# Kernel optimization log

Hardware: AMD Instinct MI355X
Metric: run time of the kernel (lower is better)

## Reference

```python
import jax, jax.numpy as jnp
import numpy as np

GRID_SIZE = 8
MARGIN = 1.0
NUM_NEG = 4
SOS_NEG = 8
LOSS_LAMBDA = 1.0
IMG_H, IMG_W = 960, 1280  # desc2 is the stride-GRID_SIZE feature map of this image
BIG = 5.0    # fill for radius-masked entries in FOS distance matrix (> max unit-desc dist 2)
HUGE = 1e6   # fill for invalid entries in SOS candidate scores


def _l2n(x, eps=1e-8):
    return x / (jnp.linalg.norm(x, axis=-1, keepdims=True) + eps)


def _pdist(a, b, eps=1e-12):
    # a: B x N x C, b: B x M x C -> B x N x M euclidean distances
    sq = (jnp.sum(a * a, -1)[..., :, None] + jnp.sum(b * b, -1)[..., None, :]
          - 2.0 * jnp.einsum('bnc,bmc->bnm', a, b))
    return jnp.sqrt(jnp.maximum(sq, eps))


def _bilinear(desc, pts):
    # desc: B x C x H x W, pts: B x N x 2 in (y, x) image-pixel coords -> B x N x C
    B, C, H, W = desc.shape
    g = pts / GRID_SIZE - 0.5  # image coords -> feature-grid coords
    gy = jnp.clip(g[..., 0], 0.0, H - 1.0)
    gx = jnp.clip(g[..., 1], 0.0, W - 1.0)
    y0 = jnp.clip(jnp.floor(gy).astype(jnp.int32), 0, H - 2)
    x0 = jnp.clip(jnp.floor(gx).astype(jnp.int32), 0, W - 2)
    wy = (gy - y0)[:, None, :]
    wx = (gx - x0)[:, None, :]
    flat = desc.reshape(B, C, H * W)
    gat = lambda yi, xi: jnp.take_along_axis(flat, (yi * W + xi)[:, None, :], axis=2)
    v00, v01 = gat(y0, x0), gat(y0, x0 + 1)
    v10, v11 = gat(y0 + 1, x0), gat(y0 + 1, x0 + 1)
    out = (v00 * (1 - wy) * (1 - wx) + v01 * (1 - wy) * wx
           + v10 * wy * (1 - wx) + v11 * wy * wx)
    return out.transpose(0, 2, 1)


def _forward(kp1, w_kp1, kp1_desc, desc2, homo12):
    r = 2.0 * GRID_SIZE  # spatial masking radius
    d1 = _l2n(kp1_desc)                       # B x N x C
    w_desc = _l2n(_bilinear(desc2, w_kp1))    # B x N x C interpolated warped descriptors

    # visibility of kp1 under homography homo12 (kp stored as (y, x))
    ones = jnp.ones_like(kp1[..., :1])
    p = jnp.concatenate([kp1[..., 1:2], kp1[..., 0:1], ones], -1)  # (x, y, 1)
    q = jnp.einsum('bij,bnj->bni', homo12, p)
    qx = q[..., 0] / (q[..., 2] + 1e-8)
    qy = q[..., 1] / (q[..., 2] + 1e-8)
    vis = ((qx >= 0) & (qx < IMG_W) & (qy >= 0) & (qy < IMG_H)).astype(d1.dtype)
    denom = jnp.sum(vis) + 1e-8

    # ---- FOS: hard quad triplet with radius masking ----
    pos = jnp.sqrt(jnp.sum((d1 - w_desc) ** 2, -1) + 1e-12)  # B x N
    D = _pdist(d1, w_desc)          # B x N x N cross descriptor distances
    s22 = _pdist(w_kp1, w_kp1)      # B x N x N warped-coordinate distances
    Dm = jnp.where(s22 <= r, BIG, D)  # mask spatial near-positives (incl. diagonal)
    neg1 = -jax.lax.top_k(-Dm, NUM_NEG)[0]                       # hardest negs per row anchor
    neg2 = -jax.lax.top_k(-Dm.transpose(0, 2, 1), NUM_NEG)[0]    # per column anchor
    t1 = jnp.mean(jax.nn.relu(MARGIN + pos[..., None] - neg1), -1)
    t2 = jnp.mean(jax.nn.relu(MARGIN + pos[..., None] - neg2), -1)
    fos = jnp.sum(vis * 0.5 * (t1 + t2)) / denom

    # ---- SOS: radius-masked second-order similarity regularizer ----
    s11 = _pdist(kp1, kp1)
    d11 = _pdist(d1, d1)
    d22 = _pdist(w_desc, w_desc)
    valid = (s11 > r) & (s22 > r)
    score = jnp.where(valid, d11, HUGE)
    nscore, idx = jax.lax.top_k(-score, SOS_NEG)  # sos_neg hardest valid neighbors
    sel_d11 = -nscore
    sel_d22 = jnp.take_along_axis(d22, idx, axis=2)
    diff2 = jnp.where(sel_d11 < HUGE * 0.1, (sel_d11 - sel_d22) ** 2, 0.0)
    sos_i = jnp.sqrt(jnp.sum(diff2, -1) + 1e-12)
    sos = jnp.sum(vis * sos_i) / denom

    return (fos + sos) * LOSS_LAMBDA


def setup_inputs() -> dict:
    key = jax.random.key(0)
    k1, k2, k3, k4, k5 = jax.random.split(key, 5)
    B, N, C, H, W = 2, 4096, 128, 120, 160
    scale = jnp.array([IMG_H - 1.0, IMG_W - 1.0], dtype=jnp.float32)
    kp1 = jax.random.uniform(k1, (B, N, 2), dtype=jnp.float32) * scale
    w_kp1 = jax.random.uniform(k2, (B, N, 2), dtype=jnp.float32) * scale
    kp1_desc = jax.random.normal(k3, (B, N, C), dtype=jnp.float32)
    desc2 = jax.random.normal(k4, (B, C, H, W), dtype=jnp.float32)
    homo12 = (jnp.tile(jnp.eye(3, dtype=jnp.float32), (B, 1, 1))
              + 0.001 * jax.random.normal(k5, (B, 3, 3), dtype=jnp.float32))
    return {'kp1': kp1, 'w_kp1': w_kp1, 'kp1_desc': kp1_desc,
            'desc2': desc2, 'homo12': homo12}


def reference(kp1, w_kp1, kp1_desc, desc2, homo12):
    return _forward(kp1, w_kp1, kp1_desc, desc2, homo12)
```

## Files before the change

### kernel.cpp

```cpp
#include <hip/hip_runtime.h>
#include <hip/hip_fp16.h>
#include <math.h>

#define NPTS 4096
#define CDIM 128
#define FH 120
#define FW 160
#define PIX (FH * FW)

typedef __attribute__((ext_vector_type(8))) short short8_t;
typedef __attribute__((ext_vector_type(4))) float float4_t;
typedef __attribute__((ext_vector_type(2))) unsigned short ushort2_t;

#define OFF_FRAG  0
#define OFF_WDB   1048576
#define OFF_JA    1572864
#define OFF_JB    1605632
#define OFF_POS   1622016
#define OFF_VIS   1630208
#define OFF_ACC   1638400
#define OFF_PARTS 1638416
#define OFF_D2T   2031632
#define OFF_END   4489232

__device__ __forceinline__ unsigned short f2bf(float f) {
  unsigned int u = __float_as_uint(f);
  u = (u + 0x7fffu + ((u >> 16) & 1u)) >> 16;
  return (unsigned short)u;
}

__device__ __forceinline__ float wavesum(float v) {
#pragma unroll
  for (int off = 1; off < 64; off <<= 1) v += __shfl_xor(v, off, 64);
  return v;
}

__global__ __launch_bounds__(256) void transpose_desc2(
    const float* __restrict__ d2, unsigned short* __restrict__ out) {
  __shared__ unsigned short tile[64][130];
  const int bp = blockIdx.x;
  const int b = bp / 300;
  const int p0 = (bp - b * 300) * 64;
  const int tid = threadIdx.x;
  const int grp = tid >> 6, lp = tid & 63;
#pragma unroll 4
  for (int r = 0; r < 32; ++r) {
    int c = (r << 2) | grp;
    float v = d2[((size_t)b * CDIM + c) * PIX + p0 + lp];
    tile[lp][c] = __half_as_ushort(__float2half(v));
  }
  __syncthreads();
  unsigned int* ob = (unsigned int*)(out + ((size_t)b * PIX + p0) * CDIM);
#pragma unroll
  for (int i = 0; i < 16; ++i) {
    int u = (i << 8) | tid;
    int p = u >> 6, cc = (u & 63) << 1;
    unsigned int lo = tile[p][cc], hi = tile[p][cc + 1];
    ob[u] = lo | (hi << 16);
  }
}

#define PREP_TAIL() do {                                                        \
  {                                                                             \
    const int T = (p & (NPTS - 1)) >> 4, cRow = p & 15;                         \
    const int kcL = lane >> 4, quadL = (lane >> 2) & 3, jjL = (lane & 3) * 2;   \
    const size_t off = (size_t)(quadL * 16 + cRow) * 8 + jjL;                   \
    const size_t tb = (((size_t)b * 256 + T) * 2) * 4;                          \
    ushort2_t st; st.x = f2bf(d0); st.y = f2bf(d1v);                            \
    ushort2_t sw; sw.x = f2bf(e0); sw.y = f2bf(e1);                             \
    *(ushort2_t*)(frag + (tb + kcL) * 512 + off) = st;                          \
    *(ushort2_t*)(frag + (tb + 4 + kcL) * 512 + off) = sw;                      \
    ushort2_t swr; swr.x = f2bf(e0); swr.y = f2bf(e1);                          \
    *(ushort2_t*)(wdb + (size_t)p * CDIM + c2) = swr;                           \
  }                                                                             \
  float dd0 = d0 - e0, dd1 = d1v - e1;                                          \
  float ssp = wavesum(dd0 * dd0 + dd1 * dd1);                                   \
  if (lane == 0) {                                                              \
    pos[p] = sqrtf(ssp + 1e-12f);                                               \
    float ky = kp1[p * 2 + 0], kx = kp1[p * 2 + 1];                             \
    jA[p] = make_float4(ky, kx, y, x);                                          \
    jB[p] = make_float2(n1, n2);                                                \
    const float* h = homo + b * 9;                                              \
    float t0 = h[0] * kx + h[1] * ky + h[2];                                    \
    float t1 = h[3] * kx + h[4] * ky + h[5];                                    \
    float t2 = h[6] * kx + h[7] * ky + h[8];                                    \
    float qx = t0 / (t2 + 1e-8f), qy = t1 / (t2 + 1e-8f);                       \
    vis[p] = (qx >= 0.0f && qx < 1280.0f && qy >= 0.0f && qy < 960.0f)          \
                 ? 1.0f : 0.0f;                                                 \
  }                                                                             \
} while (0)

__global__ __launch_bounds__(256) void prep_t(
    const float* __restrict__ kp1, const float* __restrict__ wkp1,
    const float* __restrict__ desc, const unsigned short* __restrict__ d2t,
    const float* __restrict__ homo,
    unsigned short* __restrict__ frag, unsigned short* __restrict__ wdb,
    float4* __restrict__ jA, float2* __restrict__ jB,
    float* __restrict__ pos, float* __restrict__ vis, float* __restrict__ acc) {
  const int tid = threadIdx.x;
  if (blockIdx.x == 0 && tid < 4) acc[tid] = 0.0f;
  const int p = blockIdx.x * 4 + (tid >> 6);
  const int lane = tid & 63;
  const int b = p >> 12;
  const int c2 = lane * 2;

  float2 v = *(const float2*)(desc + (size_t)p * CDIM + c2);
  float ss = wavesum(v.x * v.x + v.y * v.y);
  float inv = 1.0f / (sqrtf(ss) + 1e-8f);
  float d0 = v.x * inv, d1v = v.y * inv;
  float n1 = ss * inv * inv;

  float y = wkp1[p * 2 + 0], x = wkp1[p * 2 + 1];
  float gy = fminf(fmaxf(y * 0.125f - 0.5f, 0.0f), (float)(FH - 1));
  float gx = fminf(fmaxf(x * 0.125f - 0.5f, 0.0f), (float)(FW - 1));
  int y0 = (int)floorf(gy); y0 = min(max(y0, 0), FH - 2);
  int x0 = (int)floorf(gx); x0 = min(max(x0, 0), FW - 2);
  float wy = gy - (float)y0, wx = gx - (float)x0;
  float w00 = (1 - wy) * (1 - wx), w01 = (1 - wy) * wx;
  float w10 = wy * (1 - wx), w11 = wy * wx;
  const unsigned int* t00 = (const unsigned int*)
      (d2t + ((size_t)b * PIX + y0 * FW + x0) * CDIM) + lane;
  unsigned int u00 = t00[0], u01 = t00[64];
  unsigned int u10 = t00[FW * 64], u11 = t00[FW * 64 + 64];
  float2 f00 = __half22float2(*(const __half2*)&u00);
  float2 f01 = __half22float2(*(const __half2*)&u01);
  float2 f10 = __half22float2(*(const __half2*)&u10);
  float2 f11 = __half22float2(*(const __half2*)&u11);
  float wv0 = f00.x * w00 + f01.x * w01 + f10.x * w10 + f11.x * w11;
  float wv1 = f00.y * w00 + f01.y * w01 + f10.y * w10 + f11.y * w11;
  float ss2 = wavesum(wv0 * wv0 + wv1 * wv1);
  float inv2 = 1.0f / (sqrtf(ss2) + 1e-8f);
  float e0 = wv0 * inv2, e1 = wv1 * inv2;
  float n2 = ss2 * inv2 * inv2;

  PREP_TAIL();
}

__global__ __launch_bounds__(256) void prep_g(
    const float* __restrict__ kp1, const float* __restrict__ wkp1,
    const float* __restrict__ desc, const float* __restrict__ desc2,
    const float* __restrict__ homo,
    unsigned short* __restrict__ frag, unsigned short* __restrict__ wdb,
    float4* __restrict__ jA, float2* __restrict__ jB,
    float* __restrict__ pos, float* __restrict__ vis, float* __restrict__ acc) {
  const int tid = threadIdx.x;
  if (blockIdx.x == 0 && tid < 4) acc[tid] = 0.0f;
  const int p = blockIdx.x * 4 + (tid >> 6);
  const int lane = tid & 63;
  const int b = p >> 12;
  const int c2 = lane * 2;

  float2 v = *(const float2*)(desc + (size_t)p * CDIM + c2);
  float ss = wavesum(v.x * v.x + v.y * v.y);
  float inv = 1.0f / (sqrtf(ss) + 1e-8f);
  float d0 = v.x * inv, d1v = v.y * inv;
  float n1 = ss * inv * inv;

  float y = wkp1[p * 2 + 0], x = wkp1[p * 2 + 1];
  float gy = fminf(fmaxf(y * 0.125f - 0.5f, 0.0f), (float)(FH - 1));
  float gx = fminf(fmaxf(x * 0.125f - 0.5f, 0.0f), (float)(FW - 1));
  int y0 = (int)floorf(gy); y0 = min(max(y0, 0), FH - 2);
  int x0 = (int)floorf(gx); x0 = min(max(x0, 0), FW - 2);
  float wy = gy - (float)y0, wx = gx - (float)x0;
  float w00 = (1 - wy) * (1 - wx), w01 = (1 - wy) * wx;
  float w10 = wy * (1 - wx), w11 = wy * wx;
  const float* q0 = desc2 + ((size_t)b * CDIM + c2) * PIX + y0 * FW + x0;
  const float* q1 = q0 + PIX;
  float wv0 = q0[0] * w00 + q0[1] * w01 + q0[FW] * w10 + q0[FW + 1] * w11;
  float wv1 = q1[0] * w00 + q1[1] * w01 + q1[FW] * w10 + q1[FW + 1] * w11;
  float ss2 = wavesum(wv0 * wv0 + wv1 * wv1);
  float inv2 = 1.0f / (sqrtf(ss2) + 1e-8f);
  float e0 = wv0 * inv2, e1 = wv1 * inv2;
  float n2 = ss2 * inv2 * inv2;

  PREP_TAIL();
}

__device__ __forceinline__ void ins4m(float v, float* L) {
  float p0 = L[0]; L[0] = fmaxf(L[0], v);
  float p1 = L[1]; L[1] = __builtin_amdgcn_fmed3f(p0, L[1], v);
  float p2 = L[2]; L[2] = __builtin_amdgcn_fmed3f(p1, L[2], v);
  L[3] = __builtin_amdgcn_fmed3f(p2, L[3], v);
}
__device__ __forceinline__ void ins6m(float v, float* L) {
  float p0 = L[0]; L[0] = fmaxf(L[0], v);
  float p1 = L[1]; L[1] = __builtin_amdgcn_fmed3f(p0, L[1], v);
  float p2 = L[2]; L[2] = __builtin_amdgcn_fmed3f(p1, L[2], v);
  float p3 = L[3]; L[3] = __builtin_amdgcn_fmed3f(p2, L[3], v);
  float p4 = L[4]; L[4] = __builtin_amdgcn_fmed3f(p3, L[4], v);
  L[5] = __builtin_amdgcn_fmed3f(p4, L[5], v);
}
__device__ __forceinline__ void ins10m(float v, float* L) {
  float p0 = L[0]; L[0] = fmaxf(L[0], v);
  float pk = p0;
#pragma unroll
  for (int k = 1; k < 9; ++k) {
    float cur = L[k];
    L[k] = __builtin_amdgcn_fmed3f(pk, cur, v);
    pk = cur;
  }
  L[9] = __builtin_amdgcn_fmed3f(pk, L[9], v);
}

__device__ __forceinline__ float packkey(float s, int j) {
  return __uint_as_float((__float_as_uint(s) & 0xFFFFF000u) | (unsigned)j);
}

#define TILE_COMPUTE(AD, AW, NA, NB, J0) do {                                   \
  float4_t aD = {0,0,0,0}, aDt = {0,0,0,0}, a11 = {0,0,0,0};                    \
  _Pragma("unroll")                                                             \
  for (int kc = 0; kc < 4; ++kc) {                                              \
    aD  = __builtin_amdgcn_mfma_f32_16x16x32_bf16(AW[kc], Bd[kc], aD,  0,0,0);  \
    aDt = __builtin_amdgcn_mfma_f32_16x16x32_bf16(AD[kc], Bw[kc], aDt, 0,0,0);  \
    a11 = __builtin_amdgcn_mfma_f32_16x16x32_bf16(AD[kc], Bd[kc], a11, 0,0,0);  \
  }                                                                             \
  const float nj1[4] = {NA.x, NA.z, NB.x, NB.z};                                \
  const float nj2[4] = {NA.y, NA.w, NB.y, NB.w};                                \
  _Pragma("unroll")                                                             \
  for (int reg = 0; reg < 4; ++reg) {                                           \
    const int jj = (J0) + (quad << 2) + reg;                                    \
    ins4m(packkey(fmaf(2.0f, aD[reg],  -nj2[reg]), jj), fD);                    \
    ins4m(packkey(fmaf(2.0f, aDt[reg], -nj1[reg]), jj), fDt);                   \
    ins6m(packkey(fmaf(2.0f, a11[reg], -nj1[reg]), jj), fS);                    \
  }                                                                             \
} while (0)

__global__ __launch_bounds__(256, 3) void loss_main(
    const unsigned short* __restrict__ frag,
    const float2* __restrict__ jBg, float* __restrict__ parts) {
  __shared__ float mb[4][16][24];

  const int tid = threadIdx.x;
  const int bid = blockIdx.x;
  const int b = bid & 1;
  const int half = (bid >> 1) & 1;
  const int g = bid >> 2;
  const int i0 = g * 16;
  const int wave = tid >> 6, lane = tid & 63;
  const int c = lane & 15, quad = lane >> 4;
  const int base = b * NPTS;

  short8_t Bd[4], Bw[4];
  {
    const unsigned short* fb = frag + ((((size_t)b * 256 + g) * 2) * 4) * 512 + (size_t)lane * 8;
#pragma unroll
    for (int kc = 0; kc < 4; ++kc) {
      Bd[kc] = *(const short8_t*)(fb + kc * 512);
      Bw[kc] = *(const short8_t*)(fb + (4 + kc) * 512);
    }
  }

  float fD[4], fDt[4], fS[6];
#pragma unroll
  for (int k = 0; k < 4; ++k) { fD[k] = -1e30f; fDt[k] = -1e30f; }
#pragma unroll
  for (int k = 0; k < 6; ++k) fS[k] = -1e30f;

  const int jstart = (half << 11) | (wave << 9);
  const unsigned short* fa = frag + (((size_t)b * 256 + (jstart >> 4)) * 8) * 512 + (size_t)lane * 8;
  const float2* jbb = jBg + base;

  short8_t A0d[4], A0w[4], A1d[4], A1w[4];
#pragma unroll
  for (int kc = 0; kc < 4; ++kc) {
    A0d[kc] = *(const short8_t*)(fa + kc * 512);
    A0w[kc] = *(const short8_t*)(fa + (4 + kc) * 512);
  }
  float4 n0a = *(const float4*)(jbb + jstart + (quad << 2));
  float4 n0b = *(const float4*)(jbb + jstart + (quad << 2) + 2);
  float4 n1a, n1b;

  for (int t = 0; t < 32; t += 2) {
    const unsigned short* f1 = fa + 4096;
#pragma unroll
    for (int kc = 0; kc < 4; ++kc) {
      A1d[kc] = *(const short8_t*)(f1 + kc * 512);
      A1w[kc] = *(const short8_t*)(f1 + (4 + kc) * 512);
    }
    {
      const int j1 = jstart + ((t + 1) << 4);
      n1a = *(const float4*)(jbb + j1 + (quad << 2));
      n1b = *(const float4*)(jbb + j1 + (quad << 2) + 2);
    }
    TILE_COMPUTE(A0d, A0w, n0a, n0b, jstart + (t << 4));
    const unsigned short* f2 = fa + ((t + 2 < 32) ? 8192 : 0);
#pragma unroll
    for (int kc = 0; kc < 4; ++kc) {
      A0d[kc] = *(const short8_t*)(f2 + kc * 512);
      A0w[kc] = *(const short8_t*)(f2 + (4 + kc) * 512);
    }
    {
      const int j2 = jstart + (((t + 2) & 31) << 4);
      n0a = *(const float4*)(jbb + j2 + (quad << 2));
      n0b = *(const float4*)(jbb + j2 + (quad << 2) + 2);
    }
    TILE_COMPUTE(A1d, A1w, n1a, n1b, jstart + ((t + 1) << 4));
    fa += 8192;
  }

  float eD[6], eDt[6], eS[10];
#pragma unroll
  for (int k = 0; k < 4; ++k) { eD[k] = fD[k]; eDt[k] = fDt[k]; }
  eD[4] = eD[5] = eDt[4] = eDt[5] = -1e30f;
#pragma unroll
  for (int k = 0; k < 6; ++k) eS[k] = fS[k];
  eS[6] = eS[7] = eS[8] = eS[9] = -1e30f;

  {
    float tmp[10];
#pragma unroll
    for (int off = 16; off <= 32; off <<= 1) {
#pragma unroll
      for (int k = 0; k < 6; ++k) tmp[k] = eD[k];
#pragma unroll
      for (int k = 0; k < 6; ++k) ins6m(__shfl_xor(tmp[k], off, 64), eD);
#pragma unroll
      for (int k = 0; k < 6; ++k) tmp[k] = eDt[k];
#pragma unroll
      for (int k = 0; k < 6; ++k) ins6m(__shfl_xor(tmp[k], off, 64), eDt);
#pragma unroll
      for (int k = 0; k < 10; ++k) tmp[k] = eS[k];
#pragma unroll
      for (int k = 0; k < 10; ++k) ins10m(__shfl_xor(tmp[k], off, 64), eS);
    }
  }

#pragma unroll
  for (int h2 = 2; h2 >= 1; h2 >>= 1) {
    if (wave >= h2 && wave < 2 * h2 && lane < 16) {
      float* m = &mb[wave][lane][0];
#pragma unroll
      for (int k = 0; k < 6; ++k) { m[k] = eD[k]; m[6 + k] = eDt[k]; }
#pragma unroll
      for (int k = 0; k < 10; ++k) m[12 + k] = eS[k];
    }
    __syncthreads();
    if (wave < h2 && lane < 16) {
      const float* m = &mb[wave + h2][lane][0];
#pragma unroll
      for (int k = 0; k < 6; ++k) ins6m(m[k], eD);
#pragma unroll
      for (int k = 0; k < 6; ++k) ins6m(m[6 + k], eDt);
#pragma unroll
      for (int k = 0; k < 10; ++k) ins10m(m[12 + k], eS);
    }
  }

  if (wave == 0 && lane < 16) {
    float* P = parts + (size_t)(half * 24) * 8192 + (base + i0 + lane);
#pragma unroll
    for (int k = 0; k < 6; ++k) {
      P[(size_t)k * 8192] = eD[k];
      P[(size_t)(6 + k) * 8192] = eDt[k];
    }
#pragma unroll
    for (int k = 0; k < 10; ++k) P[(size_t)(12 + k) * 8192] = eS[k];
  }
}

__device__ __forceinline__ float bflo(unsigned int u) { return __uint_as_float(u << 16); }
__device__ __forceinline__ float bfhi(unsigned int u) { return __uint_as_float(u & 0xFFFF0000u); }

__global__ __launch_bounds__(256) void merge_filter(
    const float* __restrict__ parts, const float4* __restrict__ jAg,
    const float2* __restrict__ jBg, const float* __restrict__ posg,
    const float* __restrict__ visg, const unsigned short* __restrict__ wdb,
    float* __restrict__ accum, float* __restrict__ out) {
  __shared__ int sJ[256];
  __shared__ float sD11[256], sD22[256], sFos[32], sVis[32], sN2[32];
  const int tid = threadIdx.x;
  const int a0 = blockIdx.x * 32;

  if (tid < 32) {
    const int a = a0 + tid;
    const int base = a & ~(NPTS - 1);
    float fD[6], fDt[6], fS[10];
    const float* P = parts + a;
#pragma unroll
    for (int k = 0; k < 6; ++k) { fD[k] = P[(size_t)k * 8192]; fDt[k] = P[(size_t)(6 + k) * 8192]; }
#pragma unroll
    for (int k = 0; k < 10; ++k) fS[k] = P[(size_t)(12 + k) * 8192];
    {
      const float* Q = P + (size_t)24 * 8192;
#pragma unroll
      for (int k = 0; k < 6; ++k) {
        ins6m(Q[(size_t)k * 8192], fD);
        ins6m(Q[(size_t)(6 + k) * 8192], fDt);
      }
#pragma unroll
      for (int k = 0; k < 10; ++k) ins10m(Q[(size_t)(12 + k) * 8192], fS);
    }

    const float4 own = jAg[a];
    const float2 nb = jBg[a];
    const float pv = posg[a], vv = visg[a];
    float t1s = 0.0f, t2s = 0.0f;
    int got = 0;
#pragma unroll
    for (int k = 0; k < 6; ++k) {
      int j = (int)(__float_as_uint(fD[k]) & 0xFFFu);
      float4 jc = jAg[base + j];
      float dz = own.z - jc.z, dw = own.w - jc.w;
      if (got < 4 && dz * dz + dw * dw > 256.0f) {
        float d2 = nb.x - fD[k];
        t1s += fmaxf(1.0f + pv - sqrtf(fmaxf(d2, 1e-12f)), 0.0f);
        got++;
      }
    }
    got = 0;
#pragma unroll
    for (int k = 0; k < 6; ++k) {
      int j = (int)(__float_as_uint(fDt[k]) & 0xFFFu);
      float4 jc = jAg[base + j];
      float dz = own.z - jc.z, dw = own.w - jc.w;
      if (got < 4 && dz * dz + dw * dw > 256.0f) {
        float d2 = nb.y - fDt[k];
        t2s += fmaxf(1.0f + pv - sqrtf(fmaxf(d2, 1e-12f)), 0.0f);
        got++;
      }
    }
    int m = 0;
#pragma unroll
    for (int k = 0; k < 10; ++k) {
      int j = (int)(__float_as_uint(fS[k]) & 0xFFFu);
      float4 jc = jAg[base + j];
      float ay = own.x - jc.x, ax = own.y - jc.y;
      float wz = own.z - jc.z, ww = own.w - jc.w;
      if (m < 8 && ay * ay + ax * ax > 256.0f && wz * wz + ww * ww > 256.0f) {
        sJ[tid * 8 + m] = base + j;
        sD11[tid * 8 + m] = sqrtf(fmaxf(nb.x - fS[k], 1e-12f));
        m++;
      }
    }
    for (int k = m; k < 8; ++k) sJ[tid * 8 + k] = -1;
    sFos[tid] = vv * 0.125f * (t1s + t2s);
    sVis[tid] = vv;
    sN2[tid] = nb.y;
  }
  __syncthreads();

  {
    const int slot = tid;
    const int al = slot >> 3;
    const int j = sJ[slot];
    float d22 = 0.0f;
    if (j >= 0) {
      const uint4* pi = (const uint4*)(wdb + (size_t)(a0 + al) * CDIM);
      const uint4* pj = (const uint4*)(wdb + (size_t)j * CDIM);
      float dot = 0.0f;
#pragma unroll
      for (int qq = 0; qq < 16; ++qq) {
        uint4 ui = pi[qq], uj = pj[qq];
        dot = fmaf(bflo(ui.x), bflo(uj.x), dot); dot = fmaf(bfhi(ui.x), bfhi(uj.x), dot);
        dot = fmaf(bflo(ui.y), bflo(uj.y), dot); dot = fmaf(bfhi(ui.y), bfhi(uj.y), dot);
        dot = fmaf(bflo(ui.z), bflo(uj.z), dot); dot = fmaf(bfhi(ui.z), bfhi(uj.z), dot);
        dot = fmaf(bflo(ui.w), bflo(uj.w), dot); dot = fmaf(bfhi(ui.w), bfhi(uj.w), dot);
      }
      d22 = sqrtf(fmaxf(sN2[al] + jBg[j].y - 2.0f * dot, 1e-12f));
    }
    sD22[slot] = d22;
  }
  __syncthreads();

  float contrib = 0.0f, vsum = 0.0f;
  if (tid < 32) {
    float s = 0.0f;
#pragma unroll
    for (int k = 0; k < 8; ++k) {
      if (sJ[tid * 8 + k] >= 0) {
        float d = sD11[tid * 8 + k] - sD22[tid * 8 + k];
        s = fmaf(d, d, s);
      }
    }
    contrib = sFos[tid] + sVis[tid] * sqrtf(s + 1e-12f);
    vsum = sVis[tid];
  }
  if (tid < 64) {
#pragma unroll
    for (int off = 32; off >= 1; off >>= 1) {
      contrib += __shfl_down(contrib, off, 64);
      vsum += __shfl_down(vsum, off, 64);
    }
    if (tid == 0) {
      atomicAdd(&accum[0], contrib);
      atomicAdd(&accum[1], vsum);
      __threadfence();
      float old = atomicAdd(&accum[2], 1.0f);
      if (old == 255.0f) {
        float t = atomicAdd(&accum[0], 0.0f);
        float v = atomicAdd(&accum[1], 0.0f);
        out[0] = t / (v + 1e-8f);
      }
    }
  }
}

extern "C" void kernel_launch(void* const* d_in, const int* in_sizes, int n_in,
                              void* d_out, int out_size, void* d_ws, size_t ws_size,
                              hipStream_t stream) {
  (void)in_sizes; (void)n_in; (void)out_size;
  const float* kp1   = (const float*)d_in[0];
  const float* wkp1  = (const float*)d_in[1];
  const float* desc  = (const float*)d_in[2];
  const float* desc2 = (const float*)d_in[3];
  const float* homo  = (const float*)d_in[4];
  float* ws = (float*)d_ws;
  unsigned short* frag = (unsigned short*)(ws + OFF_FRAG);
  unsigned short* wdb  = (unsigned short*)(ws + OFF_WDB);
  float4* jA = (float4*)(ws + OFF_JA);
  float2* jB = (float2*)(ws + OFF_JB);
  float* pos = ws + OFF_POS;
  float* vis = ws + OFF_VIS;
  float* acc = ws + OFF_ACC;
  float* parts = ws + OFF_PARTS;
  unsigned short* d2t = (unsigned short*)(ws + OFF_D2T);

  if (ws_size >= (size_t)OFF_END * 4) {
    transpose_desc2<<<600, 256, 0, stream>>>(desc2, d2t);
    prep_t<<<2048, 256, 0, stream>>>(kp1, wkp1, desc, d2t, homo,
                                     frag, wdb, jA, jB, pos, vis, acc);
  } else {
    prep_g<<<2048, 256, 0, stream>>>(kp1, wkp1, desc, desc2, homo,
                                     frag, wdb, jA, jB, pos, vis, acc);
  }
  loss_main<<<1024, 256, 0, stream>>>(frag, jB, parts);
  merge_filter<<<256, 256, 0, stream>>>(parts, jA, jB, pos, vis, wdb, acc,
                                        (float*)d_out);
}
```

Measured before the change: 169.5 us.

## Fuse merge into loss_main with last-arriver reduction and LDS double-buffered j-tiles

The main kernel now splits the j dimension into 8 segments per 64-row group. Each block stages the shared j-fragment tiles into LDS through global_load_lds DMA with a double buffer, where before every wave read them straight from global memory. The cross-wave LDS merge and the separate merge_filter launch are removed. A per-tile atomic counter lets the last segment to finish merge all partial top-k lists and run the filter and SOS work inline, which saves a kernel launch and lets tiles share loaded fragments. In exchange it adds a __syncthreads per tile, more partial-result traffic (8 segments), serialized tail work in the last-arriving blocks, and a change of occupancy hint from 3 to 4.

```diff
diff --git a/kernel.cpp b/kernel.cpp
--- a/kernel.cpp
+++ b/kernel.cpp
@@ -7,6 +7,7 @@
 #define FH 120
 #define FW 160
 #define PIX (FH * FW)
+#define SEGS 8
 
 typedef __attribute__((ext_vector_type(8))) short short8_t;
 typedef __attribute__((ext_vector_type(4))) float float4_t;
@@ -19,9 +20,17 @@
 #define OFF_POS   1622016
 #define OFF_VIS   1630208
 #define OFF_ACC   1638400
-#define OFF_PARTS 1638416
-#define OFF_D2T   2031632
-#define OFF_END   4489232
+#define OFF_CNT   1638416
+#define OFF_PARTS 1638928
+#define OFF_D2T   3080720
+#define OFF_END   4309520
+
+typedef const __attribute__((address_space(1))) unsigned int* gas_ptr_t;
+typedef __attribute__((address_space(3))) unsigned int* las_ptr_t;
+
+__device__ __forceinline__ void dma16(const void* g, void* l) {
+  __builtin_amdgcn_global_load_lds((gas_ptr_t)g, (las_ptr_t)l, 16, 0, 0);
+}
 
 __device__ __forceinline__ unsigned short f2bf(float f) {
   unsigned int u = __float_as_uint(f);
@@ -90,15 +99,21 @@
   }                                                                             \
 } while (0)
 
+#define PREP_INIT() do {                                                        \
+  if (blockIdx.x < 2) cnt[blockIdx.x * 256 + tid] = 0;                          \
+  if (blockIdx.x == 2 && tid < 8) acc[tid] = 0.0f;                              \
+} while (0)
+
 __global__ __launch_bounds__(256) void prep_t(
     const float* __restrict__ kp1, const float* __restrict__ wkp1,
     const float* __restrict__ desc, const unsigned short* __restrict__ d2t,
     const float* __restrict__ homo,
     unsigned short* __restrict__ frag, unsigned short* __restrict__ wdb,
     float4* __restrict__ jA, float2* __restrict__ jB,
-    float* __restrict__ pos, float* __restrict__ vis, float* __restrict__ acc) {
+    float* __restrict__ pos, float* __restrict__ vis,
+    float* __restrict__ acc, int* __restrict__ cnt) {
   const int tid = threadIdx.x;
-  if (blockIdx.x == 0 && tid < 4) acc[tid] = 0.0f;
+  PREP_INIT();
   const int p = blockIdx.x * 4 + (tid >> 6);
   const int lane = tid & 63;
   const int b = p >> 12;
@@ -142,9 +157,10 @@
     const float* __restrict__ homo,
     unsigned short* __restrict__ frag, unsigned short* __restrict__ wdb,
     float4* __restrict__ jA, float2* __restrict__ jB,
-    float* __restrict__ pos, float* __restrict__ vis, float* __restrict__ acc) {
+    float* __restrict__ pos, float* __restrict__ vis,
+    float* __restrict__ acc, int* __restrict__ cnt) {
   const int tid = threadIdx.x;
-  if (blockIdx.x == 0 && tid < 4) acc[tid] = 0.0f;
+  PREP_INIT();
   const int p = blockIdx.x * 4 + (tid >> 6);
   const int lane = tid & 63;
   const int b = p >> 12;
@@ -206,43 +222,32 @@
   return __uint_as_float((__float_as_uint(s) & 0xFFFFF000u) | (unsigned)j);
 }
 
-#define TILE_COMPUTE(AD, AW, NA, NB, J0) do {                                   \
-  float4_t aD = {0,0,0,0}, aDt = {0,0,0,0}, a11 = {0,0,0,0};                    \
-  _Pragma("unroll")                                                             \
-  for (int kc = 0; kc < 4; ++kc) {                                              \
-    aD  = __builtin_amdgcn_mfma_f32_16x16x32_bf16(AW[kc], Bd[kc], aD,  0,0,0);  \
-    aDt = __builtin_amdgcn_mfma_f32_16x16x32_bf16(AD[kc], Bw[kc], aDt, 0,0,0);  \
-    a11 = __builtin_amdgcn_mfma_f32_16x16x32_bf16(AD[kc], Bd[kc], a11, 0,0,0);  \
-  }                                                                             \
-  const float nj1[4] = {NA.x, NA.z, NB.x, NB.z};                                \
-  const float nj2[4] = {NA.y, NA.w, NB.y, NB.w};                                \
-  _Pragma("unroll")                                                             \
-  for (int reg = 0; reg < 4; ++reg) {                                           \
-    const int jj = (J0) + (quad << 2) + reg;                                    \
-    ins4m(packkey(fmaf(2.0f, aD[reg],  -nj2[reg]), jj), fD);                    \
-    ins4m(packkey(fmaf(2.0f, aDt[reg], -nj1[reg]), jj), fDt);                   \
-    ins6m(packkey(fmaf(2.0f, a11[reg], -nj1[reg]), jj), fS);                    \
-  }                                                                             \
-} while (0)
-
-__global__ __launch_bounds__(256, 3) void loss_main(
+__device__ __forceinline__ float bflo(unsigned int u) { return __uint_as_float(u << 16); }
+__device__ __forceinline__ float bfhi(unsigned int u) { return __uint_as_float(u & 0xFFFF0000u); }
+
+__global__ __launch_bounds__(256, 4) void loss_main(
     const unsigned short* __restrict__ frag,
-    const float2* __restrict__ jBg, float* __restrict__ parts) {
-  __shared__ float mb[4][16][24];
+    const float4* __restrict__ jAg, const float2* __restrict__ jBg,
+    const float* __restrict__ posg, const float* __restrict__ visg,
+    const unsigned short* __restrict__ wdb,
+    float* __restrict__ parts, int* __restrict__ cnt,
+    float* __restrict__ accum, float* __restrict__ out) {
+  __shared__ char ldsA[2][8192];
 
   const int tid = threadIdx.x;
   const int bid = blockIdx.x;
   const int b = bid & 1;
-  const int half = (bid >> 1) & 1;
-  const int g = bid >> 2;
-  const int i0 = g * 16;
+  const int seg = (bid >> 1) & 7;
+  const int grp = bid >> 4;
   const int wave = tid >> 6, lane = tid & 63;
-  const int c = lane & 15, quad = lane >> 4;
+  const int atile = grp * 4 + wave;
+  const int i0 = atile * 16;
+  const int quad = lane >> 4;
   const int base = b * NPTS;
 
   short8_t Bd[4], Bw[4];
   {
-    const unsigned short* fb = frag + ((((size_t)b * 256 + g) * 2) * 4) * 512 + (size_t)lane * 8;
+    const unsigned short* fb = frag + (((size_t)b * 256 + atile) * 8) * 512 + (size_t)lane * 8;
 #pragma unroll
     for (int kc = 0; kc < 4; ++kc) {
       Bd[kc] = *(const short8_t*)(fb + kc * 512);
@@ -256,46 +261,57 @@
 #pragma unroll
   for (int k = 0; k < 6; ++k) fS[k] = -1e30f;
 
-  const int jstart = (half << 11) | (wave << 9);
-  const unsigned short* fa = frag + (((size_t)b * 256 + (jstart >> 4)) * 8) * 512 + (size_t)lane * 8;
-  const float2* jbb = jBg + base;
-
-  short8_t A0d[4], A0w[4], A1d[4], A1w[4];
-#pragma unroll
-  for (int kc = 0; kc < 4; ++kc) {
-    A0d[kc] = *(const short8_t*)(fa + kc * 512);
-    A0w[kc] = *(const short8_t*)(fa + (4 + kc) * 512);
-  }
-  float4 n0a = *(const float4*)(jbb + jstart + (quad << 2));
-  float4 n0b = *(const float4*)(jbb + jstart + (quad << 2) + 2);
-  float4 n1a, n1b;
-
-  for (int t = 0; t < 32; t += 2) {
-    const unsigned short* f1 = fa + 4096;
+  const int jstart = seg << 9;
+  const unsigned short* ft = frag + (((size_t)b * 256 + (jstart >> 4)) * 8) * 512;
+
+  {
+    const unsigned short* tb0 = ft;
+#pragma unroll
+    for (int ch = 0; ch < 2; ++ch) {
+      int chunk = wave * 2 + ch;
+      dma16(tb0 + chunk * 512 + lane * 8, &ldsA[0][chunk * 1024]);
+    }
+  }
+  __syncthreads();
+
+  for (int t = 0; t < 32; ++t) {
+    const int cur = t & 1;
+    if (t + 1 < 32) {
+      const unsigned short* tbn = ft + (size_t)(t + 1) * 4096;
+#pragma unroll
+      for (int ch = 0; ch < 2; ++ch) {
+        int chunk = wave * 2 + ch;
+        dma16(tbn + chunk * 512 + lane * 8, &ldsA[cur ^ 1][chunk * 1024]);
+      }
+    }
+    const char* lb = &ldsA[cur][0];
+    short8_t Ad[4], Aw[4];
 #pragma unroll
     for (int kc = 0; kc < 4; ++kc) {
-      A1d[kc] = *(const short8_t*)(f1 + kc * 512);
-      A1w[kc] = *(const short8_t*)(f1 + (4 + kc) * 512);
-    }
-    {
-      const int j1 = jstart + ((t + 1) << 4);
-      n1a = *(const float4*)(jbb + j1 + (quad << 2));
-      n1b = *(const float4*)(jbb + j1 + (quad << 2) + 2);
-    }
-    TILE_COMPUTE(A0d, A0w, n0a, n0b, jstart + (t << 4));
-    const unsigned short* f2 = fa + ((t + 2 < 32) ? 8192 : 0);
+      Ad[kc] = *(const short8_t*)(lb + kc * 1024 + lane * 16);
+      Aw[kc] = *(const short8_t*)(lb + (4 + kc) * 1024 + lane * 16);
+    }
+    const int j0 = jstart + (t << 4);
+    const float4 nA = *(const float4*)(jBg + base + j0 + (quad << 2));
+    const float4 nB = *(const float4*)(jBg + base + j0 + (quad << 2) + 2);
+
+    float4_t aD = {0, 0, 0, 0}, aDt = {0, 0, 0, 0}, a11 = {0, 0, 0, 0};
 #pragma unroll
     for (int kc = 0; kc < 4; ++kc) {
-      A0d[kc] = *(const short8_t*)(f2 + kc * 512);
-      A0w[kc] = *(const short8_t*)(f2 + (4 + kc) * 512);
-    }
-    {
-      const int j2 = jstart + (((t + 2) & 31) << 4);
-      n0a = *(const float4*)(jbb + j2 + (quad << 2));
-      n0b = *(const float4*)(jbb + j2 + (quad << 2) + 2);
-    }
-    TILE_COMPUTE(A1d, A1w, n1a, n1b, jstart + ((t + 1) << 4));
-    fa += 8192;
+      aD  = __builtin_amdgcn_mfma_f32_16x16x32_bf16(Aw[kc], Bd[kc], aD,  0, 0, 0);
+      aDt = __builtin_amdgcn_mfma_f32_16x16x32_bf16(Ad[kc], Bw[kc], aDt, 0, 0, 0);
+      a11 = __builtin_amdgcn_mfma_f32_16x16x32_bf16(Ad[kc], Bd[kc], a11, 0, 0, 0);
+    }
+    const float nj1[4] = {nA.x, nA.z, nB.x, nB.z};
+    const float nj2[4] = {nA.y, nA.w, nB.y, nB.w};
+#pragma unroll
+    for (int reg = 0; reg < 4; ++reg) {
+      const int jj = j0 + (quad << 2) + reg;
+      ins4m(packkey(fmaf(2.0f, aD[reg],  -nj2[reg]), jj), fD);
+      ins4m(packkey(fmaf(2.0f, aDt[reg], -nj1[reg]), jj), fDt);
+      ins6m(packkey(fmaf(2.0f, a11[reg], -nj1[reg]), jj), fS);
+    }
+    __syncthreads();
   }
 
   float eD[6], eDt[6], eS[10];
@@ -305,7 +321,6 @@
 #pragma unroll
   for (int k = 0; k < 6; ++k) eS[k] = fS[k];
   eS[6] = eS[7] = eS[8] = eS[9] = -1e30f;
-
   {
     float tmp[10];
 #pragma unroll
@@ -325,29 +340,9 @@
     }
   }
 
-#pragma unroll
-  for (int h2 = 2; h2 >= 1; h2 >>= 1) {
-    if (wave >= h2 && wave < 2 * h2 && lane < 16) {
-      float* m = &mb[wave][lane][0];
-#pragma unroll
-      for (int k = 0; k < 6; ++k) { m[k] = eD[k]; m[6 + k] = eDt[k]; }
-#pragma unroll
-      for (int k = 0; k < 10; ++k) m[12 + k] = eS[k];
-    }
-    __syncthreads();
-    if (wave < h2 && lane < 16) {
-      const float* m = &mb[wave + h2][lane][0];
-#pragma unroll
-      for (int k = 0; k < 6; ++k) ins6m(m[k], eD);
-#pragma unroll
-      for (int k = 0; k < 6; ++k) ins6m(m[6 + k], eDt);
-#pragma unroll
-      for (int k = 0; k < 10; ++k) ins10m(m[12 + k], eS);
-    }
-  }
-
-  if (wave == 0 && lane < 16) {
-    float* P = parts + (size_t)(half * 24) * 8192 + (base + i0 + lane);
+  if (lane < 16) {
+    const int a = base + i0 + lane;
+    float* P = parts + (size_t)(seg * 22) * 8192 + a;
 #pragma unroll
     for (int k = 0; k < 6; ++k) {
       P[(size_t)k * 8192] = eD[k];
@@ -356,41 +351,35 @@
 #pragma unroll
     for (int k = 0; k < 10; ++k) P[(size_t)(12 + k) * 8192] = eS[k];
   }
-}
-
-__device__ __forceinline__ float bflo(unsigned int u) { return __uint_as_float(u << 16); }
-__device__ __forceinline__ float bfhi(unsigned int u) { return __uint_as_float(u & 0xFFFF0000u); }
-
-__global__ __launch_bounds__(256) void merge_filter(
-    const float* __restrict__ parts, const float4* __restrict__ jAg,
-    const float2* __restrict__ jBg, const float* __restrict__ posg,
-    const float* __restrict__ visg, const unsigned short* __restrict__ wdb,
-    float* __restrict__ accum, float* __restrict__ out) {
-  __shared__ int sJ[256];
-  __shared__ float sD11[256], sD22[256], sFos[32], sVis[32], sN2[32];
-  const int tid = threadIdx.x;
-  const int a0 = blockIdx.x * 32;
-
-  if (tid < 32) {
-    const int a = a0 + tid;
-    const int base = a & ~(NPTS - 1);
-    float fD[6], fDt[6], fS[10];
-    const float* P = parts + a;
-#pragma unroll
-    for (int k = 0; k < 6; ++k) { fD[k] = P[(size_t)k * 8192]; fDt[k] = P[(size_t)(6 + k) * 8192]; }
-#pragma unroll
-    for (int k = 0; k < 10; ++k) fS[k] = P[(size_t)(12 + k) * 8192];
-    {
-      const float* Q = P + (size_t)24 * 8192;
+  __threadfence();
+  int old = 0;
+  if (lane == 0) old = atomicAdd(&cnt[b * 256 + atile], 1);
+  old = __shfl(old, 0, 64);
+  if (old != SEGS - 1) return;
+  __threadfence();
+
+  char* scr = &ldsA[0][wave * 2048];
+  int*   sJ   = (int*)scr;
+  float* sD11 = (float*)(scr + 512);
+  float* sD22 = (float*)(scr + 1024);
+  float* sN2  = (float*)(scr + 1536);
+  float* sFv  = (float*)(scr + 1600);
+  float* sVv  = (float*)(scr + 1664);
+
+  if (lane < 16) {
+    const int a = base + i0 + lane;
+#pragma unroll
+    for (int s = 0; s < SEGS; ++s) {
+      if (s == seg) continue;
+      const float* Q = parts + (size_t)(s * 22) * 8192 + a;
 #pragma unroll
       for (int k = 0; k < 6; ++k) {
-        ins6m(Q[(size_t)k * 8192], fD);
-        ins6m(Q[(size_t)(6 + k) * 8192], fDt);
-      }
-#pragma unroll
-      for (int k = 0; k < 10; ++k) ins10m(Q[(size_t)(12 + k) * 8192], fS);
-    }
-
+        ins6m(Q[(size_t)k * 8192], eD);
+        ins6m(Q[(size_t)(6 + k) * 8192], eDt);
+      }
+#pragma unroll
+      for (int k = 0; k < 10; ++k) ins10m(Q[(size_t)(12 + k) * 8192], eS);
+    }
     const float4 own = jAg[a];
     const float2 nb = jBg[a];
     const float pv = posg[a], vv = visg[a];
@@ -398,11 +387,11 @@
     int got = 0;
 #pragma unroll
     for (int k = 0; k < 6; ++k) {
-      int j = (int)(__float_as_uint(fD[k]) & 0xFFFu);
+      int j = (int)(__float_as_uint(eD[k]) & 0xFFFu);
       float4 jc = jAg[base + j];
       float dz = own.z - jc.z, dw = own.w - jc.w;
       if (got < 4 && dz * dz + dw * dw > 256.0f) {
-        float d2 = nb.x - fD[k];
+        float d2 = nb.x - eD[k];
         t1s += fmaxf(1.0f + pv - sqrtf(fmaxf(d2, 1e-12f)), 0.0f);
         got++;
       }
@@ -410,11 +399,11 @@
     got = 0;
 #pragma unroll
     for (int k = 0; k < 6; ++k) {
-      int j = (int)(__float_as_uint(fDt[k]) & 0xFFFu);
+      int j = (int)(__float_as_uint(eDt[k]) & 0xFFFu);
       float4 jc = jAg[base + j];
       float dz = own.z - jc.z, dw = own.w - jc.w;
       if (got < 4 && dz * dz + dw * dw > 256.0f) {
-        float d2 = nb.y - fDt[k];
+        float d2 = nb.y - eDt[k];
         t2s += fmaxf(1.0f + pv - sqrtf(fmaxf(d2, 1e-12f)), 0.0f);
         got++;
       }
@@ -422,30 +411,31 @@
     int m = 0;
 #pragma unroll
     for (int k = 0; k < 10; ++k) {
-      int j = (int)(__float_as_uint(fS[k]) & 0xFFFu);
+      int j = (int)(__float_as_uint(eS[k]) & 0xFFFu);
       float4 jc = jAg[base + j];
       float ay = own.x - jc.x, ax = own.y - jc.y;
       float wz = own.z - jc.z, ww = own.w - jc.w;
       if (m < 8 && ay * ay + ax * ax > 256.0f && wz * wz + ww * ww > 256.0f) {
-        sJ[tid * 8 + m] = base + j;
-        sD11[tid * 8 + m] = sqrtf(fmaxf(nb.x - fS[k], 1e-12f));
+        sJ[lane * 8 + m] = base + j;
+        sD11[lane * 8 + m] = sqrtf(fmaxf(nb.x - eS[k], 1e-12f));
         m++;
       }
     }
-    for (int k = m; k < 8; ++k) sJ[tid * 8 + k] = -1;
-    sFos[tid] = vv * 0.125f * (t1s + t2s);
-    sVis[tid] = vv;
-    sN2[tid] = nb.y;
-  }
-  __syncthreads();
-
-  {
-    const int slot = tid;
+    for (int k = m; k < 8; ++k) sJ[lane * 8 + k] = -1;
+    sFv[lane] = vv * 0.125f * (t1s + t2s);
+    sVv[lane] = vv;
+    sN2[lane] = nb.y;
+  }
+  asm volatile("" ::: "memory");
+
+#pragma unroll
+  for (int rep = 0; rep < 2; ++rep) {
+    const int slot = lane + rep * 64;
     const int al = slot >> 3;
     const int j = sJ[slot];
     float d22 = 0.0f;
     if (j >= 0) {
-      const uint4* pi = (const uint4*)(wdb + (size_t)(a0 + al) * CDIM);
+      const uint4* pi = (const uint4*)(wdb + (size_t)(base + i0 + al) * CDIM);
       const uint4* pj = (const uint4*)(wdb + (size_t)j * CDIM);
       float dot = 0.0f;
 #pragma unroll
@@ -460,37 +450,35 @@
     }
     sD22[slot] = d22;
   }
-  __syncthreads();
+  asm volatile("" ::: "memory");
 
   float contrib = 0.0f, vsum = 0.0f;
-  if (tid < 32) {
+  if (lane < 16) {
     float s = 0.0f;
 #pragma unroll
     for (int k = 0; k < 8; ++k) {
-      if (sJ[tid * 8 + k] >= 0) {
-        float d = sD11[tid * 8 + k] - sD22[tid * 8 + k];
+      if (sJ[lane * 8 + k] >= 0) {
+        float d = sD11[lane * 8 + k] - sD22[lane * 8 + k];
         s = fmaf(d, d, s);
       }
     }
-    contrib = sFos[tid] + sVis[tid] * sqrtf(s + 1e-12f);
-    vsum = sVis[tid];
-  }
-  if (tid < 64) {
-#pragma unroll
-    for (int off = 32; off >= 1; off >>= 1) {
-      contrib += __shfl_down(contrib, off, 64);
-      vsum += __shfl_down(vsum, off, 64);
-    }
-    if (tid == 0) {
-      atomicAdd(&accum[0], contrib);
-      atomicAdd(&accum[1], vsum);
-      __threadfence();
-      float old = atomicAdd(&accum[2], 1.0f);
-      if (old == 255.0f) {
-        float t = atomicAdd(&accum[0], 0.0f);
-        float v = atomicAdd(&accum[1], 0.0f);
-        out[0] = t / (v + 1e-8f);
-      }
+    contrib = sFv[lane] + sVv[lane] * sqrtf(s + 1e-12f);
+    vsum = sVv[lane];
+  }
+#pragma unroll
+  for (int off = 8; off >= 1; off >>= 1) {
+    contrib += __shfl_down(contrib, off, 64);
+    vsum += __shfl_down(vsum, off, 64);
+  }
+  if (lane == 0) {
+    atomicAdd(&accum[0], contrib);
+    atomicAdd(&accum[1], vsum);
+    __threadfence();
+    float o2 = atomicAdd(&accum[2], 1.0f);
+    if (o2 == 511.0f) {
+      float tt = atomicAdd(&accum[0], 0.0f);
+      float vv2 = atomicAdd(&accum[1], 0.0f);
+      out[0] = tt / (vv2 + 1e-8f);
     }
   }
 }
@@ -512,18 +500,18 @@
   float* pos = ws + OFF_POS;
   float* vis = ws + OFF_VIS;
   float* acc = ws + OFF_ACC;
+  int* cnt   = (int*)(ws + OFF_CNT);
   float* parts = ws + OFF_PARTS;
   unsigned short* d2t = (unsigned short*)(ws + OFF_D2T);
 
   if (ws_size >= (size_t)OFF_END * 4) {
     transpose_desc2<<<600, 256, 0, stream>>>(desc2, d2t);
     prep_t<<<2048, 256, 0, stream>>>(kp1, wkp1, desc, d2t, homo,
-                                     frag, wdb, jA, jB, pos, vis, acc);
+                                     frag, wdb, jA, jB, pos, vis, acc, cnt);
   } else {
     prep_g<<<2048, 256, 0, stream>>>(kp1, wkp1, desc, desc2, homo,
-                                     frag, wdb, jA, jB, pos, vis, acc);
-  }
-  loss_main<<<1024, 256, 0, stream>>>(frag, jB, parts);
-  merge_filter<<<256, 256, 0, stream>>>(parts, jA, jB, pos, vis, wdb, acc,
-                                        (float*)d_out);
-}
+                                     frag, wdb, jA, jB, pos, vis, acc, cnt);
+  }
+  loss_main<<<1024, 256, 0, stream>>>(frag, jA, jB, pos, vis, wdb,
+                                      parts, cnt, acc, (float*)d_out);
+}
```

New measurement: 300.6 us. 77.4% more time.
